# Kernel optimization log

Hardware: AMD Instinct MI355X
Metric: run time of the kernel (lower is better)

The kernel has to match this reference:

```python
import jax, jax.numpy as jnp
import numpy as np

EMB, QK, V, H = 1024, 64, 64, 16
B, S = 4, 2048


def setup_inputs() -> dict:
    key = jax.random.key(0)
    ks = jax.random.split(key, 8)
    sc = 0.02
    x_q = jax.random.normal(ks[0], (B, S, EMB), jnp.float32)
    x_k_v = jax.random.normal(ks[1], (B, S, EMB), jnp.float32)
    # causal mask: True means masked (matches torch masked_fill)
    causal = ~jnp.tril(jnp.ones((S, S), dtype=bool))
    attn_mask = jnp.broadcast_to(causal, (B, S, S))
    w_q = jax.random.normal(ks[2], (H * QK, EMB), jnp.float32) * sc
    b_q = jnp.zeros((H * QK,), jnp.float32)
    w_k = jax.random.normal(ks[3], (H * QK, EMB), jnp.float32) * sc
    b_k = jnp.zeros((H * QK,), jnp.float32)
    w_v = jax.random.normal(ks[4], (H * V, EMB), jnp.float32) * sc
    b_v = jnp.zeros((H * V,), jnp.float32)
    return {"x_q": x_q, "x_k_v": x_k_v, "attn_mask": attn_mask,
            "w_q": w_q, "b_q": b_q, "w_k": w_k, "b_k": b_k, "w_v": w_v, "b_v": b_v}


def reference(x_q, x_k_v, attn_mask, w_q, b_q, w_k, b_k, w_v, b_v):
    Bq, Sq, _ = x_q.shape
    Skv = x_k_v.shape[1]
    q = (x_q @ w_q.T + b_q).reshape(Bq, Sq, H, QK).transpose(0, 2, 1, 3)   # [B,H,Sq,QK]
    k = (x_k_v @ w_k.T + b_k).reshape(Bq, Skv, H, QK).transpose(0, 2, 1, 3)  # [B,H,Skv,QK]
    v = (x_k_v @ w_v.T + b_v).reshape(Bq, Skv, H, V).transpose(0, 2, 1, 3)   # [B,H,Skv,V]
    attn = jnp.einsum('bhqd,bhkd->bhqk', q, k) / jnp.sqrt(jnp.float32(QK))
    attn = jnp.where(attn_mask[:, None, :, :], jnp.float32(-1e9), attn)
    attn = jax.nn.softmax(attn, axis=-1)
    z = jnp.einsum('bhqk,bhkv->bhqv', attn, v)        # [B,H,Sq,V]
    z = z.transpose(0, 2, 1, 3).reshape(Bq, Sq, H * V)
    return z
```

## Files before the change

kernel.cpp:

```cpp
#include <hip/hip_runtime.h>

#define B_    4
#define H_    16
#define S_    2048
#define EMB_  1024
#define D_    64

typedef __attribute__((ext_vector_type(4))) float f32x4;
typedef __attribute__((ext_vector_type(8))) short frag_ab;
typedef unsigned short ushort_t;

__device__ __forceinline__ unsigned short f2bf(float f) {
    unsigned int u = __float_as_uint(f);
    unsigned int r = u + 0x7fffu + ((u >> 16) & 1u);
    return (unsigned short)(r >> 16);
}
__device__ __forceinline__ unsigned short f2bf_fast(float f) {
    return (unsigned short)((__float_as_uint(f) + 0x8000u) >> 16);
}

__device__ __forceinline__ void gld16(const void* g, void* l) {
    __builtin_amdgcn_global_load_lds(
        (const __attribute__((address_space(1))) void*)g,
        (__attribute__((address_space(3))) void*)l, 16, 0, 0);
}

#define SCOL(lane) ((((lane) & 7) ^ (((lane) >> 3) & 7)) * 8)

__global__ void cvt_all(const float* __restrict__ s0, const float* __restrict__ s1,
                        const float* __restrict__ s2, const float* __restrict__ s3,
                        const float* __restrict__ s4,
                        ushort_t* __restrict__ d0, ushort_t* __restrict__ d1,
                        ushort_t* __restrict__ d2, ushort_t* __restrict__ d3,
                        ushort_t* __restrict__ d4) {
    const int z = blockIdx.z;
    const float* src; ushort_t* dst; int n4;
    switch (z) {
        case 0: src = s0; dst = d0; n4 = 262144; break;
        case 1: src = s1; dst = d1; n4 = 262144; break;
        case 2: src = s2; dst = d2; n4 = 262144; break;
        case 3: src = s3; dst = d3; n4 = 2097152; break;
        default: src = s4; dst = d4; n4 = 2097152; break;
    }
    int i = blockIdx.x * blockDim.x + threadIdx.x;
    if (i >= n4) return;
    float4 f = ((const float4*)src)[i];
    ushort4 o;
    o.x = f2bf(f.x); o.y = f2bf(f.y); o.z = f2bf(f.z); o.w = f2bf(f.w);
    ((ushort4*)dst)[i] = o;
}

__global__ __launch_bounds__(256) void qkv_gemm(
    const ushort_t* __restrict__ xq,
    const ushort_t* __restrict__ xkv,
    const ushort_t* __restrict__ wq,
    const ushort_t* __restrict__ wk,
    const ushort_t* __restrict__ wv,
    const float* __restrict__ bq,
    const float* __restrict__ bk,
    const float* __restrict__ bv,
    ushort_t* __restrict__ qo,
    ushort_t* __restrict__ ko,
    ushort_t* __restrict__ vto)
{
    __shared__ ushort_t As[2][128 * 64];
    __shared__ ushort_t Bs[2][128 * 64];

    const int id = blockIdx.x;
    const int xcd = id & 7, j = id >> 3;
    const int m_t = xcd * 8 + (j & 7);
    const int n_t = (j >> 3) & 7;
    const int z   = j >> 6;

    const ushort_t* A = (z == 0) ? xq : xkv;
    const ushort_t* W = (z == 0) ? wq : (z == 1 ? wk : wv);
    const float* bias = (z == 0) ? bq : (z == 1 ? bk : bv);
    const float scale = (z == 0) ? 0.125f * 1.44269504089f : 1.0f;

    const int tid = threadIdx.x;
    const int m0 = m_t * 128, n0 = n_t * 128;
    const int w = tid >> 6, lane = tid & 63, quad = lane >> 4, l16 = lane & 15;
    const int wm = w & 1, wn = w >> 1;
    const int scol = SCOL(lane);

    f32x4 acc[4][4];
#pragma unroll
    for (int i = 0; i < 4; ++i)
#pragma unroll
        for (int j2 = 0; j2 < 4; ++j2) acc[i][j2] = (f32x4){0.f, 0.f, 0.f, 0.f};

    const ushort_t* pa = A + (size_t)(m0 + w * 32 + (lane >> 3)) * EMB_ + scol;
    const ushort_t* pw = W + (size_t)(n0 + w * 32 + (lane >> 3)) * EMB_ + scol;

    auto stage = [&](int bsel, int kt) {
        const int k0 = kt * 64;
#pragma unroll
        for (int i = 0; i < 4; ++i) {
            const int base = w * 32 + i * 8;
            gld16(pa + (size_t)(i * 8) * EMB_ + k0, &As[bsel][base * 64]);
            gld16(pw + (size_t)(i * 8) * EMB_ + k0, &Bs[bsel][base * 64]);
        }
    };

    const int key = l16 & 7;
    stage(0, 0);
    for (int kt = 0; kt < 16; ++kt) {
        __syncthreads();
        if (kt < 15) stage((kt + 1) & 1, kt + 1);
        const int bsel = kt & 1;

#pragma unroll
        for (int c = 0; c < 2; ++c) {
            const int boff = ((c * 4 + quad) ^ key) * 8;
            frag_ab a[4], bfr[4];
#pragma unroll
            for (int t = 0; t < 4; ++t) {
                a[t]   = *(const frag_ab*)&As[bsel][(wm * 64 + t * 16 + l16) * 64 + boff];
                bfr[t] = *(const frag_ab*)&Bs[bsel][(wn * 64 + t * 16 + l16) * 64 + boff];
            }
#pragma unroll
            for (int tm = 0; tm < 4; ++tm)
#pragma unroll
                for (int tn = 0; tn < 4; ++tn)
                    acc[tm][tn] = __builtin_amdgcn_mfma_f32_16x16x32_bf16(
                        a[tm], bfr[tn], acc[tm][tn], 0, 0, 0);
        }
    }

    if (z == 2) {
#pragma unroll
        for (int tn = 0; tn < 4; ++tn) {
            int n = n0 + wn * 64 + tn * 16 + l16;
            float bval = bias[n];
            int hh = n >> 6, dd = n & 63;
#pragma unroll
            for (int tm = 0; tm < 4; ++tm) {
                int m = m0 + wm * 64 + tm * 16 + quad * 4;
                int bb = m >> 11, ss = m & (S_ - 1);
                union { ushort4 v; ushort_t u[4]; } pk;
#pragma unroll
                for (int r = 0; r < 4; ++r) pk.u[r] = f2bf(acc[tm][tn][r] + bval);
                *(ushort4*)&vto[(((size_t)bb * H_ + hh) * D_ + dd) * S_ + ss] = pk.v;
            }
        }
    } else {
        ushort_t* ob = (z == 0) ? qo : ko;
#pragma unroll
        for (int tn = 0; tn < 4; ++tn) {
            int n = n0 + wn * 64 + tn * 16 + l16;
            float bval = bias[n];
            int hh = n >> 6, dd = n & 63;
#pragma unroll
            for (int tm = 0; tm < 4; ++tm) {
#pragma unroll
                for (int r = 0; r < 4; ++r) {
                    int m = m0 + wm * 64 + tm * 16 + quad * 4 + r;
                    int bb = m >> 11, ss = m & (S_ - 1);
                    float val = (acc[tm][tn][r] + bval) * scale;
                    ob[(((size_t)bb * H_ + hh) * S_ + ss) * D_ + dd] = f2bf(val);
                }
            }
        }
    }
}

__global__ __launch_bounds__(256) void attn_kernel(
    const ushort_t* __restrict__ qg,
    const ushort_t* __restrict__ kg,
    const ushort_t* __restrict__ vtg,
    float* __restrict__ out)
{
    __shared__ ushort_t Kt[2][64 * 64];
    __shared__ ushort_t Vt[2][64 * 64];
    __shared__ ushort_t Pb[4][32 * 64];

    const int tid = threadIdx.x;
    const int w = tid >> 6, lane = tid & 63, quad = lane >> 4, l16 = lane & 15;
    const int scol = SCOL(lane);

    const int id = blockIdx.x;
    const int rr = id >> 3;
    const int bh = (id & 7) + 8 * (rr & 7);
    const int qi = 15 - (rr >> 3);
    const int q0 = qi * 128;
    const int b = bh >> 4, h = bh & 15;

    const ushort_t* qp  = qg  + (size_t)bh * S_ * D_;
    const ushort_t* kp  = kg  + (size_t)bh * S_ * D_;
    const ushort_t* vtp = vtg + (size_t)bh * D_ * S_;

    frag_ab aq[2][2];
#pragma unroll
    for (int rg = 0; rg < 2; ++rg) {
        const ushort_t* qr = qp + (size_t)(q0 + rg * 64 + w * 16 + l16) * D_;
        aq[rg][0] = *(const frag_ab*)(qr + quad * 8);
        aq[rg][1] = *(const frag_ab*)(qr + 32 + quad * 8);
    }

    float psum[2][4];
    f32x4 o[2][4];
#pragma unroll
    for (int rg = 0; rg < 2; ++rg)
#pragma unroll
        for (int r = 0; r < 4; ++r) psum[rg][r] = 0.f;
#pragma unroll
    for (int rg = 0; rg < 2; ++rg)
#pragma unroll
        for (int t = 0; t < 4; ++t) o[rg][t] = (f32x4){0.f, 0.f, 0.f, 0.f};

    ushort_t* Pw = &Pb[w][0];
    const int last = 2 * qi + 1;

    auto stage = [&](int bsel, int kt) {
#pragma unroll
        for (int i = 0; i < 2; ++i) {
            const int base = w * 16 + i * 8;
            gld16(kp  + (size_t)(kt * 64 + base + (lane >> 3)) * D_ + scol,
                  &Kt[bsel][base * 64]);
            gld16(vtp + (size_t)(base + (lane >> 3)) * S_ + kt * 64 + scol,
                  &Vt[bsel][base * 64]);
        }
    };

    const int key = l16 & 7;
    stage(0, 0);
    for (int kt = 0; kt <= last; ++kt) {
        __syncthreads();
        if (kt < last) stage((kt + 1) & 1, kt + 1);
        const int bsel = kt & 1;

        frag_ab bk[4][2], bv[4][2];
#pragma unroll
        for (int t = 0; t < 4; ++t) {
#pragma unroll
            for (int hf = 0; hf < 2; ++hf) {
                const int off = (t * 16 + l16) * 64 + ((hf * 4 + quad) ^ key) * 8;
                bk[t][hf] = *(const frag_ab*)&Kt[bsel][off];
                bv[t][hf] = *(const frag_ab*)&Vt[bsel][off];
            }
        }

#pragma unroll
        for (int rg = 0; rg < 2; ++rg) {
            if (rg == 0 && kt == last) continue;
            const bool diag = (kt == 2 * qi + rg);
            f32x4 scf[4];
#pragma unroll
            for (int tn = 0; tn < 4; ++tn) {
                f32x4 sc = (f32x4){0.f, 0.f, 0.f, 0.f};
                sc = __builtin_amdgcn_mfma_f32_16x16x32_bf16(aq[rg][0], bk[tn][0], sc, 0, 0, 0);
                sc = __builtin_amdgcn_mfma_f32_16x16x32_bf16(aq[rg][1], bk[tn][1], sc, 0, 0, 0);
                scf[tn] = sc;
            }
            if (diag) {
#pragma unroll
                for (int tn = 0; tn < 4; ++tn) {
                    int kcol = kt * 64 + tn * 16 + l16;
#pragma unroll
                    for (int r = 0; r < 4; ++r) {
                        int qrow = q0 + rg * 64 + w * 16 + quad * 4 + r;
                        if (kcol > qrow) scf[tn][r] = -1e30f;
                    }
                }
            }
#pragma unroll
            for (int r = 0; r < 4; ++r) {
                const int prow = rg * 16 + quad * 4 + r;
                const int rowoff = prow * 64 + (l16 & 7);
                const int pkey = prow & 7;
#pragma unroll
                for (int tn = 0; tn < 4; ++tn) {
                    float p = __builtin_amdgcn_exp2f(scf[tn][r]);
                    psum[rg][r] += p;
                    Pw[rowoff + ((tn * 2 + (l16 >> 3)) ^ pkey) * 8] = f2bf_fast(p);
                }
            }
        }
        asm volatile("s_waitcnt lgkmcnt(0)" ::: "memory");
#pragma unroll
        for (int rg = 0; rg < 2; ++rg) {
            if (rg == 0 && kt == last) continue;
            const int poff = (rg * 16 + l16) * 64;
            frag_ab ap0 = *(const frag_ab*)&Pw[poff + ((0 + quad) ^ key) * 8];
            frag_ab ap1 = *(const frag_ab*)&Pw[poff + ((4 + quad) ^ key) * 8];
#pragma unroll
            for (int tv = 0; tv < 4; ++tv) {
                o[rg][tv] = __builtin_amdgcn_mfma_f32_16x16x32_bf16(ap0, bv[tv][0], o[rg][tv], 0, 0, 0);
                o[rg][tv] = __builtin_amdgcn_mfma_f32_16x16x32_bf16(ap1, bv[tv][1], o[rg][tv], 0, 0, 0);
            }
        }
    }

    float* ob = out + (size_t)b * S_ * (H_ * D_) + h * D_;
#pragma unroll
    for (int rg = 0; rg < 2; ++rg) {
#pragma unroll
        for (int r = 0; r < 4; ++r) {
            float s = psum[rg][r];
            s += __shfl_xor(s, 1);
            s += __shfl_xor(s, 2);
            s += __shfl_xor(s, 4);
            s += __shfl_xor(s, 8);
            float inv = 1.0f / s;
            int srow = q0 + rg * 64 + w * 16 + quad * 4 + r;
#pragma unroll
            for (int tv = 0; tv < 4; ++tv)
                ob[(size_t)srow * (H_ * D_) + tv * 16 + l16] = o[rg][tv][r] * inv;
        }
    }
}

extern "C" void kernel_launch(void* const* d_in, const int* in_sizes, int n_in,
                              void* d_out, int out_size, void* d_ws, size_t ws_size,
                              hipStream_t stream) {
    const float* x_q  = (const float*)d_in[0];
    const float* x_kv = (const float*)d_in[1];
    const float* w_q  = (const float*)d_in[3];
    const float* b_q  = (const float*)d_in[4];
    const float* w_k  = (const float*)d_in[5];
    const float* b_k  = (const float*)d_in[6];
    const float* w_v  = (const float*)d_in[7];
    const float* b_v  = (const float*)d_in[8];
    float* out = (float*)d_out;

    ushort_t* ws  = (ushort_t*)d_ws;
    ushort_t* wqb = ws;
    ushort_t* wkb = wqb + 1048576;
    ushort_t* wvb = wkb + 1048576;
    ushort_t* xqb  = wvb + 1048576;
    ushort_t* xkvb = xqb + 8388608;
    ushort_t* qb   = xkvb + 8388608;
    ushort_t* kb   = qb + 8388608;
    ushort_t* vtb  = kb + 8388608;

    cvt_all<<<dim3(8192, 1, 5), 256, 0, stream>>>(
        w_q, w_k, w_v, x_q, x_kv, wqb, wkb, wvb, xqb, xkvb);
    qkv_gemm<<<1536, 256, 0, stream>>>(
        xqb, xkvb, wqb, wkb, wvb, b_q, b_k, b_v, qb, kb, vtb);
    attn_kernel<<<1024, 256, 0, stream>>>(qb, kb, vtb, out);
}
```

Baseline: 291.6 us.

## Rewrite attention with 32x32 MFMA, register-resident P, and paired causal tiles

The attention kernel now uses 32x32x16 bf16 MFMAs and computes S transposed (K as the A operand), so the exponentiated probabilities can be packed with cvt_pk_bf16 and rearranged with permlane32_swap straight into A-operand fragments. This removes the per-warp LDS round trip for P. Work is also rebalanced: each block pairs a low and a high 64-row query tile across its warps, so causal work evens out. The cost is that warps on the short tile sit idle through later iterations but still join the barriers. It also adds s_setprio hints around the MFMA sections and relies on gfx950-specific instructions.

```diff
diff --git a/kernel.cpp b/kernel.cpp
--- a/kernel.cpp
+++ b/kernel.cpp
@@ -7,6 +7,7 @@
 #define D_    64
 
 typedef __attribute__((ext_vector_type(4))) float f32x4;
+typedef __attribute__((ext_vector_type(16))) float f32x16;
 typedef __attribute__((ext_vector_type(8))) short frag_ab;
 typedef unsigned short ushort_t;
 
@@ -172,44 +173,36 @@
 {
     __shared__ ushort_t Kt[2][64 * 64];
     __shared__ ushort_t Vt[2][64 * 64];
-    __shared__ ushort_t Pb[4][32 * 64];
 
     const int tid = threadIdx.x;
-    const int w = tid >> 6, lane = tid & 63, quad = lane >> 4, l16 = lane & 15;
+    const int w = tid >> 6, lane = tid & 63;
+    const int hi = lane >> 5, n32 = lane & 31;
     const int scol = SCOL(lane);
+    const int key = n32 & 7;
 
     const int id = blockIdx.x;
-    const int rr = id >> 3;
-    const int bh = (id & 7) + 8 * (rr & 7);
-    const int qi = 15 - (rr >> 3);
-    const int q0 = qi * 128;
-    const int b = bh >> 4, h = bh & 15;
+    const int bh = (id & 7) + 8 * ((id >> 3) & 7);
+    const int pi = id >> 6;
+    const int reg64 = (w < 2) ? pi : (31 - pi);
+    const int qbase = reg64 * 64 + (w & 1) * 32;
+    const int lastw = reg64;
+    const int last  = 31 - pi;
 
     const ushort_t* qp  = qg  + (size_t)bh * S_ * D_;
     const ushort_t* kp  = kg  + (size_t)bh * S_ * D_;
     const ushort_t* vtp = vtg + (size_t)bh * D_ * S_;
 
-    frag_ab aq[2][2];
-#pragma unroll
-    for (int rg = 0; rg < 2; ++rg) {
-        const ushort_t* qr = qp + (size_t)(q0 + rg * 64 + w * 16 + l16) * D_;
-        aq[rg][0] = *(const frag_ab*)(qr + quad * 8);
-        aq[rg][1] = *(const frag_ab*)(qr + 32 + quad * 8);
-    }
-
-    float psum[2][4];
-    f32x4 o[2][4];
-#pragma unroll
-    for (int rg = 0; rg < 2; ++rg)
-#pragma unroll
-        for (int r = 0; r < 4; ++r) psum[rg][r] = 0.f;
-#pragma unroll
-    for (int rg = 0; rg < 2; ++rg)
-#pragma unroll
-        for (int t = 0; t < 4; ++t) o[rg][t] = (f32x4){0.f, 0.f, 0.f, 0.f};
-
-    ushort_t* Pw = &Pb[w][0];
-    const int last = 2 * qi + 1;
+    frag_ab aq[4];
+    {
+        const ushort_t* qr = qp + (size_t)(qbase + n32) * D_ + hi * 8;
+#pragma unroll
+        for (int c = 0; c < 4; ++c) aq[c] = *(const frag_ab*)(qr + c * 16);
+    }
+
+    f32x16 o0, o1;
+#pragma unroll
+    for (int r = 0; r < 16; ++r) { o0[r] = 0.f; o1[r] = 0.f; }
+    float psum = 0.f;
 
     auto stage = [&](int bsel, int kt) {
 #pragma unroll
@@ -222,91 +215,78 @@
         }
     };
 
-    const int key = l16 & 7;
     stage(0, 0);
     for (int kt = 0; kt <= last; ++kt) {
         __syncthreads();
         if (kt < last) stage((kt + 1) & 1, kt + 1);
+        if (kt > lastw) continue;
         const int bsel = kt & 1;
 
-        frag_ab bk[4][2], bv[4][2];
-#pragma unroll
-        for (int t = 0; t < 4; ++t) {
-#pragma unroll
-            for (int hf = 0; hf < 2; ++hf) {
-                const int off = (t * 16 + l16) * 64 + ((hf * 4 + quad) ^ key) * 8;
-                bk[t][hf] = *(const frag_ab*)&Kt[bsel][off];
-                bv[t][hf] = *(const frag_ab*)&Vt[bsel][off];
+        f32x16 sa0, sa1;
+#pragma unroll
+        for (int r = 0; r < 16; ++r) { sa0[r] = 0.f; sa1[r] = 0.f; }
+        __builtin_amdgcn_s_setprio(1);
+#pragma unroll
+        for (int c = 0; c < 4; ++c) {
+            frag_ab k0 = *(const frag_ab*)&Kt[bsel][(n32)      * 64 + (((2*c + hi) ^ key) * 8)];
+            frag_ab k1 = *(const frag_ab*)&Kt[bsel][(32 + n32) * 64 + (((2*c + hi) ^ key) * 8)];
+            sa0 = __builtin_amdgcn_mfma_f32_32x32x16_bf16(k0, aq[c], sa0, 0, 0, 0);
+            sa1 = __builtin_amdgcn_mfma_f32_32x32x16_bf16(k1, aq[c], sa1, 0, 0, 0);
+        }
+        __builtin_amdgcn_s_setprio(0);
+
+        const bool diag = (kt == lastw);
+        const int limbase = qbase + n32 - kt * 64 - 4 * hi;
+
+        frag_ab apk[2][2];
+#pragma unroll
+        for (int tn = 0; tn < 2; ++tn) {
+            const int lim = limbase - tn * 32;
+            unsigned pw[8];
+#pragma unroll
+            for (int r2 = 0; r2 < 8; ++r2) {
+                float plo = __builtin_amdgcn_exp2f((tn == 0) ? sa0[2*r2]   : sa1[2*r2]);
+                float phi = __builtin_amdgcn_exp2f((tn == 0) ? sa0[2*r2+1] : sa1[2*r2+1]);
+                if (diag) {
+                    const int sl = 2 * (r2 & 1) + 8 * (r2 >> 1);
+                    plo = (sl     <= lim) ? plo : 0.f;
+                    phi = (sl + 1 <= lim) ? phi : 0.f;
+                }
+                psum += plo + phi;
+                asm("v_cvt_pk_bf16_f32 %0, %1, %2" : "=v"(pw[r2]) : "v"(plo), "v"(phi));
             }
-        }
-
-#pragma unroll
-        for (int rg = 0; rg < 2; ++rg) {
-            if (rg == 0 && kt == last) continue;
-            const bool diag = (kt == 2 * qi + rg);
-            f32x4 scf[4];
-#pragma unroll
-            for (int tn = 0; tn < 4; ++tn) {
-                f32x4 sc = (f32x4){0.f, 0.f, 0.f, 0.f};
-                sc = __builtin_amdgcn_mfma_f32_16x16x32_bf16(aq[rg][0], bk[tn][0], sc, 0, 0, 0);
-                sc = __builtin_amdgcn_mfma_f32_16x16x32_bf16(aq[rg][1], bk[tn][1], sc, 0, 0, 0);
-                scf[tn] = sc;
-            }
-            if (diag) {
-#pragma unroll
-                for (int tn = 0; tn < 4; ++tn) {
-                    int kcol = kt * 64 + tn * 16 + l16;
-#pragma unroll
-                    for (int r = 0; r < 4; ++r) {
-                        int qrow = q0 + rg * 64 + w * 16 + quad * 4 + r;
-                        if (kcol > qrow) scf[tn][r] = -1e30f;
-                    }
-                }
-            }
-#pragma unroll
-            for (int r = 0; r < 4; ++r) {
-                const int prow = rg * 16 + quad * 4 + r;
-                const int rowoff = prow * 64 + (l16 & 7);
-                const int pkey = prow & 7;
-#pragma unroll
-                for (int tn = 0; tn < 4; ++tn) {
-                    float p = __builtin_amdgcn_exp2f(scf[tn][r]);
-                    psum[rg][r] += p;
-                    Pw[rowoff + ((tn * 2 + (l16 >> 3)) ^ pkey) * 8] = f2bf_fast(p);
-                }
-            }
-        }
-        asm volatile("s_waitcnt lgkmcnt(0)" ::: "memory");
-#pragma unroll
-        for (int rg = 0; rg < 2; ++rg) {
-            if (rg == 0 && kt == last) continue;
-            const int poff = (rg * 16 + l16) * 64;
-            frag_ab ap0 = *(const frag_ab*)&Pw[poff + ((0 + quad) ^ key) * 8];
-            frag_ab ap1 = *(const frag_ab*)&Pw[poff + ((4 + quad) ^ key) * 8];
-#pragma unroll
-            for (int tv = 0; tv < 4; ++tv) {
-                o[rg][tv] = __builtin_amdgcn_mfma_f32_16x16x32_bf16(ap0, bv[tv][0], o[rg][tv], 0, 0, 0);
-                o[rg][tv] = __builtin_amdgcn_mfma_f32_16x16x32_bf16(ap1, bv[tv][1], o[rg][tv], 0, 0, 0);
-            }
-        }
-    }
-
-    float* ob = out + (size_t)b * S_ * (H_ * D_) + h * D_;
-#pragma unroll
-    for (int rg = 0; rg < 2; ++rg) {
-#pragma unroll
-        for (int r = 0; r < 4; ++r) {
-            float s = psum[rg][r];
-            s += __shfl_xor(s, 1);
-            s += __shfl_xor(s, 2);
-            s += __shfl_xor(s, 4);
-            s += __shfl_xor(s, 8);
-            float inv = 1.0f / s;
-            int srow = q0 + rg * 64 + w * 16 + quad * 4 + r;
-#pragma unroll
-            for (int tv = 0; tv < 4; ++tv)
-                ob[(size_t)srow * (H_ * D_) + tv * 16 + l16] = o[rg][tv][r] * inv;
-        }
+            asm("v_permlane32_swap_b32 %0, %1" : "+v"(pw[0]), "+v"(pw[2]));
+            asm("v_permlane32_swap_b32 %0, %1" : "+v"(pw[1]), "+v"(pw[3]));
+            asm("v_permlane32_swap_b32 %0, %1" : "+v"(pw[4]), "+v"(pw[6]));
+            asm("v_permlane32_swap_b32 %0, %1" : "+v"(pw[5]), "+v"(pw[7]));
+            union { unsigned u[4]; frag_ab f; } u0, u1;
+            u0.u[0] = pw[0]; u0.u[1] = pw[1]; u0.u[2] = pw[2]; u0.u[3] = pw[3];
+            u1.u[0] = pw[4]; u1.u[1] = pw[5]; u1.u[2] = pw[6]; u1.u[3] = pw[7];
+            apk[tn][0] = u0.f;
+            apk[tn][1] = u1.f;
+        }
+
+        __builtin_amdgcn_s_setprio(1);
+#pragma unroll
+        for (int c16 = 0; c16 < 4; ++c16) {
+            frag_ab v0 = *(const frag_ab*)&Vt[bsel][(n32)      * 64 + (((2*c16 + hi) ^ key) * 8)];
+            frag_ab v1 = *(const frag_ab*)&Vt[bsel][(32 + n32) * 64 + (((2*c16 + hi) ^ key) * 8)];
+            o0 = __builtin_amdgcn_mfma_f32_32x32x16_bf16(apk[c16 >> 1][c16 & 1], v0, o0, 0, 0, 0);
+            o1 = __builtin_amdgcn_mfma_f32_32x32x16_bf16(apk[c16 >> 1][c16 & 1], v1, o1, 0, 0, 0);
+        }
+        __builtin_amdgcn_s_setprio(0);
+    }
+
+    float fs = psum + __shfl_xor(psum, 32);
+    float inv = 1.0f / fs;
+    float* ob = out + (size_t)(bh >> 4) * S_ * (H_ * D_) + (bh & 15) * D_;
+#pragma unroll
+    for (int r = 0; r < 16; ++r) {
+        const int ql = (r & 3) + 8 * (r >> 2) + 4 * hi;
+        const float iv = __shfl(inv, ql);
+        float* orow = ob + (size_t)(qbase + ql) * (H_ * D_);
+        orow[n32]      = o0[r] * iv;
+        orow[32 + n32] = o1[r] * iv;
     }
 }
 
```

New measurement: 304.9 us. +4.6%, slower.

## Fuse activation bf16 conversion into QKV GEMM A-tile loading

Applied to the files above, without the earlier changes.

Removes the separate conversion pass for x_q and x_kv. The QKV GEMM now reads the fp32 activations directly into registers, converts them with packed bf16 convert instructions and writes them into the swizzled LDS tile. Register prefetch overlaps with the MFMA loop of the current tile. This drops a full read/write round trip of the activations, but the GEMM now reads twice as many A bytes per tile and uses more registers.

```diff
diff --git a/kernel.cpp b/kernel.cpp
--- a/kernel.cpp
+++ b/kernel.cpp
@@ -27,23 +27,15 @@
 
 #define SCOL(lane) ((((lane) & 7) ^ (((lane) >> 3) & 7)) * 8)
 
-__global__ void cvt_all(const float* __restrict__ s0, const float* __restrict__ s1,
-                        const float* __restrict__ s2, const float* __restrict__ s3,
-                        const float* __restrict__ s4,
-                        ushort_t* __restrict__ d0, ushort_t* __restrict__ d1,
-                        ushort_t* __restrict__ d2, ushort_t* __restrict__ d3,
-                        ushort_t* __restrict__ d4) {
-    const int z = blockIdx.z;
-    const float* src; ushort_t* dst; int n4;
-    switch (z) {
-        case 0: src = s0; dst = d0; n4 = 262144; break;
-        case 1: src = s1; dst = d1; n4 = 262144; break;
-        case 2: src = s2; dst = d2; n4 = 262144; break;
-        case 3: src = s3; dst = d3; n4 = 2097152; break;
-        default: src = s4; dst = d4; n4 = 2097152; break;
-    }
-    int i = blockIdx.x * blockDim.x + threadIdx.x;
-    if (i >= n4) return;
+__global__ void cvt_w(const float* __restrict__ s0, const float* __restrict__ s1,
+                      const float* __restrict__ s2,
+                      ushort_t* __restrict__ d0, ushort_t* __restrict__ d1,
+                      ushort_t* __restrict__ d2) {
+    const int b = blockIdx.x;
+    const int z = b >> 10;
+    const int i = (b & 1023) * 256 + threadIdx.x;
+    const float* src = (z == 0) ? s0 : (z == 1 ? s1 : s2);
+    ushort_t* dst    = (z == 0) ? d0 : (z == 1 ? d1 : d2);
     float4 f = ((const float4*)src)[i];
     ushort4 o;
     o.x = f2bf(f.x); o.y = f2bf(f.y); o.z = f2bf(f.z); o.w = f2bf(f.w);
@@ -51,8 +43,8 @@
 }
 
 __global__ __launch_bounds__(256) void qkv_gemm(
-    const ushort_t* __restrict__ xq,
-    const ushort_t* __restrict__ xkv,
+    const float* __restrict__ xq,
+    const float* __restrict__ xkv,
     const ushort_t* __restrict__ wq,
     const ushort_t* __restrict__ wk,
     const ushort_t* __restrict__ wv,
@@ -72,7 +64,7 @@
     const int n_t = (j >> 3) & 7;
     const int z   = j >> 6;
 
-    const ushort_t* A = (z == 0) ? xq : xkv;
+    const float* A = (z == 0) ? xq : xkv;
     const ushort_t* W = (z == 0) ? wq : (z == 1 ? wk : wv);
     const float* bias = (z == 0) ? bq : (z == 1 ? bk : bv);
     const float scale = (z == 0) ? 0.125f * 1.44269504089f : 1.0f;
@@ -89,24 +81,50 @@
 #pragma unroll
         for (int j2 = 0; j2 < 4; ++j2) acc[i][j2] = (f32x4){0.f, 0.f, 0.f, 0.f};
 
-    const ushort_t* pa = A + (size_t)(m0 + w * 32 + (lane >> 3)) * EMB_ + scol;
+    const float*    pa = A + (size_t)(m0 + w * 32 + (lane >> 3)) * EMB_ + scol;
     const ushort_t* pw = W + (size_t)(n0 + w * 32 + (lane >> 3)) * EMB_ + scol;
 
-    auto stage = [&](int bsel, int kt) {
+    float4 areg[4][2];
+    auto loadA = [&](int kt) {
+        const int k0 = kt * 64;
+#pragma unroll
+        for (int i = 0; i < 4; ++i) {
+            const float* p = pa + (size_t)(i * 8) * EMB_ + k0;
+            areg[i][0] = *(const float4*)p;
+            areg[i][1] = *(const float4*)(p + 4);
+        }
+    };
+    auto writeA = [&](int bsel) {
+#pragma unroll
+        for (int i = 0; i < 4; ++i) {
+            unsigned q0, q1, q2, q3;
+            asm("v_cvt_pk_bf16_f32 %0, %1, %2" : "=v"(q0) : "v"(areg[i][0].x), "v"(areg[i][0].y));
+            asm("v_cvt_pk_bf16_f32 %0, %1, %2" : "=v"(q1) : "v"(areg[i][0].z), "v"(areg[i][0].w));
+            asm("v_cvt_pk_bf16_f32 %0, %1, %2" : "=v"(q2) : "v"(areg[i][1].x), "v"(areg[i][1].y));
+            asm("v_cvt_pk_bf16_f32 %0, %1, %2" : "=v"(q3) : "v"(areg[i][1].z), "v"(areg[i][1].w));
+            uint4 d; d.x = q0; d.y = q1; d.z = q2; d.w = q3;
+            *(uint4*)&As[bsel][(w * 32 + i * 8) * 64 + lane * 8] = d;
+        }
+    };
+    auto stageB = [&](int bsel, int kt) {
         const int k0 = kt * 64;
 #pragma unroll
         for (int i = 0; i < 4; ++i) {
             const int base = w * 32 + i * 8;
-            gld16(pa + (size_t)(i * 8) * EMB_ + k0, &As[bsel][base * 64]);
             gld16(pw + (size_t)(i * 8) * EMB_ + k0, &Bs[bsel][base * 64]);
         }
     };
 
     const int key = l16 & 7;
-    stage(0, 0);
+    loadA(0);
+    stageB(0, 0);
+    writeA(0);
     for (int kt = 0; kt < 16; ++kt) {
         __syncthreads();
-        if (kt < 15) stage((kt + 1) & 1, kt + 1);
+        if (kt < 15) {
+            loadA(kt + 1);
+            stageB((kt + 1) & 1, kt + 1);
+        }
         const int bsel = kt & 1;
 
 #pragma unroll
@@ -125,6 +143,7 @@
                     acc[tm][tn] = __builtin_amdgcn_mfma_f32_16x16x32_bf16(
                         a[tm], bfr[tn], acc[tm][tn], 0, 0, 0);
         }
+        if (kt < 15) writeA((kt + 1) & 1);
     }
 
     if (z == 2) {
@@ -327,15 +346,12 @@
     ushort_t* wqb = ws;
     ushort_t* wkb = wqb + 1048576;
     ushort_t* wvb = wkb + 1048576;
-    ushort_t* xqb  = wvb + 1048576;
-    ushort_t* xkvb = xqb + 8388608;
-    ushort_t* qb   = xkvb + 8388608;
+    ushort_t* qb   = wvb + 1048576;
     ushort_t* kb   = qb + 8388608;
     ushort_t* vtb  = kb + 8388608;
 
-    cvt_all<<<dim3(8192, 1, 5), 256, 0, stream>>>(
-        w_q, w_k, w_v, x_q, x_kv, wqb, wkb, wvb, xqb, xkvb);
+    cvt_w<<<3072, 256, 0, stream>>>(w_q, w_k, w_v, wqb, wkb, wvb);
     qkv_gemm<<<1536, 256, 0, stream>>>(
-        xqb, xkvb, wqb, wkb, wvb, b_q, b_k, b_v, qb, kb, vtb);
+        x_q, x_kv, wqb, wkb, wvb, b_q, b_k, b_v, qb, kb, vtb);
     attn_kernel<<<1024, 256, 0, stream>>>(qb, kb, vtb, out);
 }
```

New measurement: 299.0 us. 2.5% more time.

## Compact conversion grid, transpose Q/K GEMM for vector stores, add MFMA priority

Applied to the files above, without the earlier changes.

The conversion kernel now uses a flat 1D grid sized to the real work, so it no longer launches the many idle blocks the old z-indexed grid created for the smaller weight tensors. The Q/K projection swaps its operands (weights as A, activations as B), which lets the epilogue write four consecutive head-dim elements as one ushort4 and load the bias as a float4, replacing scattered 2-byte stores. The attention kernel wraps its MFMA sections in s_setprio to favour matrix issue across waves. The operand swap changes the tile mapping and L2 reuse pattern, which could hurt locality.

```diff
diff --git a/kernel.cpp b/kernel.cpp
--- a/kernel.cpp
+++ b/kernel.cpp
@@ -33,17 +33,20 @@
                         ushort_t* __restrict__ d0, ushort_t* __restrict__ d1,
                         ushort_t* __restrict__ d2, ushort_t* __restrict__ d3,
                         ushort_t* __restrict__ d4) {
-    const int z = blockIdx.z;
-    const float* src; ushort_t* dst; int n4;
-    switch (z) {
-        case 0: src = s0; dst = d0; n4 = 262144; break;
-        case 1: src = s1; dst = d1; n4 = 262144; break;
-        case 2: src = s2; dst = d2; n4 = 262144; break;
-        case 3: src = s3; dst = d3; n4 = 2097152; break;
-        default: src = s4; dst = d4; n4 = 2097152; break;
-    }
-    int i = blockIdx.x * blockDim.x + threadIdx.x;
-    if (i >= n4) return;
+    const int b = blockIdx.x;
+    const float* src; ushort_t* dst; int i;
+    if (b < 3072) {
+        const int z = b >> 10;
+        src = (z == 0) ? s0 : (z == 1 ? s1 : s2);
+        dst = (z == 0) ? d0 : (z == 1 ? d1 : d2);
+        i = (b & 1023) * 256 + threadIdx.x;
+    } else {
+        const int b2 = b - 3072;
+        const int z = b2 >> 13;
+        src = z ? s4 : s3;
+        dst = z ? d4 : d3;
+        i = (b2 & 8191) * 256 + threadIdx.x;
+    }
     float4 f = ((const float4*)src)[i];
     ushort4 o;
     o.x = f2bf(f.x); o.y = f2bf(f.y); o.z = f2bf(f.z); o.w = f2bf(f.w);
@@ -68,29 +71,37 @@
 
     const int id = blockIdx.x;
     const int xcd = id & 7, j = id >> 3;
-    const int m_t = xcd * 8 + (j & 7);
-    const int n_t = (j >> 3) & 7;
-    const int z   = j >> 6;
-
-    const ushort_t* A = (z == 0) ? xq : xkv;
-    const ushort_t* W = (z == 0) ? wq : (z == 1 ? wk : wv);
+    const int big_t   = xcd * 8 + (j & 7);
+    const int small_t = (j >> 3) & 7;
+    const int z       = j >> 6;
+
     const float* bias = (z == 0) ? bq : (z == 1 ? bk : bv);
     const float scale = (z == 0) ? 0.125f * 1.44269504089f : 1.0f;
 
     const int tid = threadIdx.x;
-    const int m0 = m_t * 128, n0 = n_t * 128;
     const int w = tid >> 6, lane = tid & 63, quad = lane >> 4, l16 = lane & 15;
     const int wm = w & 1, wn = w >> 1;
     const int scol = SCOL(lane);
 
+    int m0, n0;
+    const ushort_t *Aptr, *Bptr;
+    if (z == 2) {
+        m0 = big_t * 128;  n0 = small_t * 128;
+        Aptr = xkv;        Bptr = wv;
+    } else {
+        m0 = small_t * 128; n0 = big_t * 128;
+        Aptr = (z == 0) ? wq : wk;
+        Bptr = (z == 0) ? xq : xkv;
+    }
+
     f32x4 acc[4][4];
 #pragma unroll
     for (int i = 0; i < 4; ++i)
 #pragma unroll
         for (int j2 = 0; j2 < 4; ++j2) acc[i][j2] = (f32x4){0.f, 0.f, 0.f, 0.f};
 
-    const ushort_t* pa = A + (size_t)(m0 + w * 32 + (lane >> 3)) * EMB_ + scol;
-    const ushort_t* pw = W + (size_t)(n0 + w * 32 + (lane >> 3)) * EMB_ + scol;
+    const ushort_t* pa = Aptr + (size_t)(m0 + w * 32 + (lane >> 3)) * EMB_ + scol;
+    const ushort_t* pb = Bptr + (size_t)(n0 + w * 32 + (lane >> 3)) * EMB_ + scol;
 
     auto stage = [&](int bsel, int kt) {
         const int k0 = kt * 64;
@@ -98,7 +109,7 @@
         for (int i = 0; i < 4; ++i) {
             const int base = w * 32 + i * 8;
             gld16(pa + (size_t)(i * 8) * EMB_ + k0, &As[bsel][base * 64]);
-            gld16(pw + (size_t)(i * 8) * EMB_ + k0, &Bs[bsel][base * 64]);
+            gld16(pb + (size_t)(i * 8) * EMB_ + k0, &Bs[bsel][base * 64]);
         }
     };
 
@@ -146,19 +157,20 @@
     } else {
         ushort_t* ob = (z == 0) ? qo : ko;
 #pragma unroll
-        for (int tn = 0; tn < 4; ++tn) {
-            int n = n0 + wn * 64 + tn * 16 + l16;
-            float bval = bias[n];
-            int hh = n >> 6, dd = n & 63;
-#pragma unroll
-            for (int tm = 0; tm < 4; ++tm) {
-#pragma unroll
-                for (int r = 0; r < 4; ++r) {
-                    int m = m0 + wm * 64 + tm * 16 + quad * 4 + r;
-                    int bb = m >> 11, ss = m & (S_ - 1);
-                    float val = (acc[tm][tn][r] + bval) * scale;
-                    ob[(((size_t)bb * H_ + hh) * S_ + ss) * D_ + dd] = f2bf(val);
-                }
+        for (int tm = 0; tm < 4; ++tm) {
+            int mb = m0 + wm * 64 + tm * 16 + quad * 4;
+            int hh = mb >> 6, dd = mb & 63;
+            float4 bv4 = *(const float4*)&bias[mb];
+#pragma unroll
+            for (int tn = 0; tn < 4; ++tn) {
+                int n = n0 + wn * 64 + tn * 16 + l16;
+                int bb = n >> 11, ss = n & (S_ - 1);
+                union { ushort4 v; ushort_t u[4]; } pk;
+                pk.u[0] = f2bf((acc[tm][tn][0] + bv4.x) * scale);
+                pk.u[1] = f2bf((acc[tm][tn][1] + bv4.y) * scale);
+                pk.u[2] = f2bf((acc[tm][tn][2] + bv4.z) * scale);
+                pk.u[3] = f2bf((acc[tm][tn][3] + bv4.w) * scale);
+                *(ushort4*)&ob[(((size_t)bb * H_ + hh) * S_ + ss) * D_ + dd] = pk.v;
             }
         }
     }
@@ -245,6 +257,7 @@
             if (rg == 0 && kt == last) continue;
             const bool diag = (kt == 2 * qi + rg);
             f32x4 scf[4];
+            __builtin_amdgcn_s_setprio(1);
 #pragma unroll
             for (int tn = 0; tn < 4; ++tn) {
                 f32x4 sc = (f32x4){0.f, 0.f, 0.f, 0.f};
@@ -252,6 +265,7 @@
                 sc = __builtin_amdgcn_mfma_f32_16x16x32_bf16(aq[rg][1], bk[tn][1], sc, 0, 0, 0);
                 scf[tn] = sc;
             }
+            __builtin_amdgcn_s_setprio(0);
             if (diag) {
 #pragma unroll
                 for (int tn = 0; tn < 4; ++tn) {
@@ -283,11 +297,13 @@
             const int poff = (rg * 16 + l16) * 64;
             frag_ab ap0 = *(const frag_ab*)&Pw[poff + ((0 + quad) ^ key) * 8];
             frag_ab ap1 = *(const frag_ab*)&Pw[poff + ((4 + quad) ^ key) * 8];
+            __builtin_amdgcn_s_setprio(1);
 #pragma unroll
             for (int tv = 0; tv < 4; ++tv) {
                 o[rg][tv] = __builtin_amdgcn_mfma_f32_16x16x32_bf16(ap0, bv[tv][0], o[rg][tv], 0, 0, 0);
                 o[rg][tv] = __builtin_amdgcn_mfma_f32_16x16x32_bf16(ap1, bv[tv][1], o[rg][tv], 0, 0, 0);
             }
+            __builtin_amdgcn_s_setprio(0);
         }
     }
 
@@ -333,7 +349,7 @@
     ushort_t* kb   = qb + 8388608;
     ushort_t* vtb  = kb + 8388608;
 
-    cvt_all<<<dim3(8192, 1, 5), 256, 0, stream>>>(
+    cvt_all<<<19456, 256, 0, stream>>>(
         w_q, w_k, w_v, x_q, x_kv, wqb, wkb, wvb, xqb, xkvb);
     qkv_gemm<<<1536, 256, 0, stream>>>(
         xqb, xkvb, wqb, wkb, wvb, b_q, b_k, b_v, qb, kb, vtb);
```

Result: no change. 291.1 us (-0.2%).
